# Performance work log

Measured on AMD Instinct MI355X. Metric: run time of the kernel, lower is better.

## Reference

```python
import jax, jax.numpy as jnp
import numpy as np
import math
from jax import lax

KSIZE = 3
STRIDE = 1
RATE = 2
FUSE_K = 3
SCALE = 10.0
FUSE = True


def extract_image_patches(img, kernel, stride=1):
    # Faithful port of the torch helper (incl. pad_row applied to width).
    bsz, c, h, w = img.shape
    h2 = math.ceil(h / stride)
    w2 = math.ceil(w / stride)
    pad_row = (h2 - 1) * stride + kernel - h
    pad_col = (w2 - 1) * stride + kernel - w
    x = jnp.pad(img, ((0, 0), (0, 0),
                      (pad_col // 2, pad_col - pad_col // 2),
                      (pad_row // 2, pad_row - pad_row // 2)))
    H, W = x.shape[2], x.shape[3]
    nh = (H - kernel) // stride + 1
    nw = (W - kernel) // stride + 1
    parts = [x[:, :, ki:ki + (nh - 1) * stride + 1:stride,
                     kj:kj + (nw - 1) * stride + 1:stride]
             for ki in range(kernel) for kj in range(kernel)]
    p = jnp.stack(parts, axis=1)  # [b, k*k, c, nh, nw] -> flatten order (ki,kj,c)
    return p.reshape(bsz, kernel * kernel * c, nh, nw)


def setup_inputs() -> dict:
    key = jax.random.key(0)
    k1, k2 = jax.random.split(key)
    f = jax.random.normal(k1, (2, 64, 128, 128), dtype=jnp.float32)
    b = jax.random.normal(k2, (2, 64, 128, 128), dtype=jnp.float32)
    mask = jnp.zeros((2, 1, 128, 128), dtype=jnp.float32)
    return {"f": f, "b": b, "mask": mask}


def reference(f, b, mask):
    kernel = RATE * 2
    bs, cs, hs, ws = f.shape
    # raw background patches at stride=rate with kernel=2*rate
    raw_w = extract_image_patches(b, kernel, RATE * STRIDE)
    raw_w = raw_w.reshape(bs, -1, kernel, kernel, cs).transpose(0, 1, 4, 2, 3)  # [bs,L,cs,K,K]
    # nearest-neighbor downsample by rate (torch nearest: src = dst*rate)
    f_ds = f[:, :, ::RATE, ::RATE]
    b_ds = b[:, :, ::RATE, ::RATE]
    mask_ds = mask[:, :, ::RATE, ::RATE]
    ihs, iws = b_ds.shape[2], b_ds.shape[3]
    L = ihs * iws
    # ksize x ksize matching patches
    w = extract_image_patches(b_ds, KSIZE, STRIDE)
    w = w.reshape(bs, -1, KSIZE, KSIZE, cs).transpose(0, 1, 4, 2, 3)  # [bs,L,cs,3,3]
    # mask patches -> per-patch validity mm [L]
    m = extract_image_patches(mask_ds, KSIZE, STRIDE)
    m = m.reshape(bs, -1, KSIZE, KSIZE, 1).transpose(0, 2, 3, 4, 1)[0]  # [3,3,1,L]
    mm = (jnp.mean(m, axis=(0, 1, 2)) == 0.0).astype(f.dtype)  # [L]
    fuse_weight = jnp.eye(FUSE_K, dtype=f.dtype).reshape(1, 1, FUSE_K, FUSE_K)

    def per_sample(xi, wi, raw_wi):
        # xi [cs,ihs,iws], wi [L,cs,3,3], raw_wi [L,cs,K,K]
        norm = jnp.sqrt(jnp.sum(wi * wi, axis=(1, 2, 3)))
        wi_normed = wi / jnp.minimum(norm, 1e-4)[:, None, None, None]  # clamp(max=1e-4), faithful
        yi = lax.conv_general_dilated(xi[None], wi_normed, (1, 1), [(1, 1), (1, 1)])  # [1,L,ihs,iws]
        if FUSE:
            yi = yi.reshape(1, 1, ihs * iws, ihs * iws)
            yi = lax.conv_general_dilated(yi, fuse_weight, (1, 1), [(1, 1), (1, 1)])
            yi = yi.reshape(1, ihs, iws, ihs, iws).transpose(0, 2, 1, 4, 3)
            yi = yi.reshape(1, 1, ihs * iws, ihs * iws)
            yi = lax.conv_general_dilated(yi, fuse_weight, (1, 1), [(1, 1), (1, 1)])
            yi = yi.reshape(1, iws, ihs, iws, ihs).transpose(0, 2, 1, 4, 3)
        yi = yi.reshape(1, ihs, iws, iws * ihs)
        yi = jax.nn.softmax(yi * mm * SCALE, axis=3) * mm
        offset = jnp.argmax(yi, axis=3).astype(jnp.int32)
        offset = jnp.stack([offset // hs, offset % hs], axis=-1).transpose(0, 3, 1, 2)  # [1,2,ihs,iws]
        yi_t = yi.transpose(0, 3, 1, 2)  # [1,L,ihs,iws]
        # conv_transpose2d(yi_t, raw_wi, stride=rate, padding=1) via lhs dilation
        w_t = jnp.flip(raw_wi, axis=(-2, -1)).transpose(1, 0, 2, 3)  # [cs,L,K,K]
        pad = kernel - 1 - 1
        out = lax.conv_general_dilated(yi_t, w_t, (1, 1), [(pad, pad), (pad, pad)],
                                       lhs_dilation=(RATE, RATE)) / 4.0  # [1,cs,hs,ws]
        return out[0], offset[0]

    y, offsets = jax.vmap(per_sample)(f_ds, w, raw_w)
    h_add = jnp.broadcast_to(jnp.arange(ihs, dtype=offsets.dtype).reshape(1, 1, ihs, 1), (bs, 1, ihs, iws))
    w_add = jnp.broadcast_to(jnp.arange(iws, dtype=offsets.dtype).reshape(1, 1, 1, iws), (bs, 1, ihs, iws))
    offsets = offsets - jnp.concatenate([h_add, w_add], axis=1)
    return y, offsets
```

## Files before the change

### kernel.cpp

```cpp
#include <hip/hip_runtime.h>
#include <math.h>

#define NS   4096
#define KCH  576
#define CH   64
#define HF   128
#define HD   64
#define PLANE (NS*KCH)
#define IMG  (CH*HF*HF)

typedef __attribute__((ext_vector_type(8))) _Float16 half8;
typedef __attribute__((ext_vector_type(4))) float f32x4;

__device__ __forceinline__ int Tsw(int r){ return ((r & 63) << 6) | (r >> 6); }

typedef __attribute__((address_space(1))) unsigned int gu32;
typedef __attribute__((address_space(3))) unsigned int lu32;
__device__ __forceinline__ void gload16(const void* g, void* l){
  __builtin_amdgcn_global_load_lds((const gu32*)g, (lu32*)l, 16, 0, 0);
}

__global__ void k_mm(const float* __restrict__ mask, float* __restrict__ mm){
  int n = blockIdx.x * blockDim.x + threadIdx.x;
  if(n >= NS) return;
  float sum = 0.f;
  #pragma unroll
  for(int r9 = 0; r9 < 9; ++r9){
    int idx = n * 9 + r9;
    int p   = idx >> 12;
    int rem = idx & 4095;
    int y = rem >> 6, x = rem & 63;
    int ki = p / 3, kj = p % 3;
    int Y = ki + y - 1, X = kj + x - 1;
    float v = 0.f;
    if(Y >= 0 && Y < HD && X >= 0 && X < HD)
      v = mask[(2*Y) * HF + 2*X];
    sum += v;
  }
  mm[n] = ((sum / 9.0f) == 0.0f) ? 1.0f : 0.0f;
}

__global__ void k_WX(const float* __restrict__ f, const float* __restrict__ b,
                     _Float16* __restrict__ Wp, _Float16* __restrict__ Xp){
  int e0 = blockIdx.x * 256 + threadIdx.x;
  int samp = e0 / (2*PLANE);
  int ew = e0 - samp * (2*PLANE);
  const float* fp = f + (size_t)samp * IMG;
  const float* bp = b + (size_t)samp * IMG;
  _Float16* Wps = Wp + (size_t)samp * (2*PLANE);
  _Float16* Xps = Xp + (size_t)samp * (2*PLANE);
  if(ew < PLANE){
    int e = ew;
    int n = e / KCH, k = e - n * KCH;
    int c2 = k / 9, r9 = k - c2 * 9;
    int t = n * 9 + r9;
    int y = t & 63, ch = (t >> 6) & 63, p = t >> 12;
    int ki = p / 3, kj = p - ki * 3;
    int Y = ki + y - 1, X = kj + c2 - 1;
    float v = 0.f;
    if((unsigned)Y < 64u && (unsigned)X < 64u)
      v = bp[ch * (HF*HF) + (Y << 8) + (X << 1)];
    v *= 9.765625f;
    _Float16 h0 = (_Float16)v;
    _Float16 h1 = (_Float16)(v - (float)h0);
    Wps[e] = h0; Wps[PLANE + e] = h1;
  } else {
    int e = ew - PLANE;
    int s = e / KCH, k = e - s * KCH;
    int c2 = k / 9, r9 = k - c2 * 9, a = r9 / 3, bb = r9 - a * 3;
    int i = s >> 6, j = s & 63;
    int Y = i + a - 1, Xc = j + bb - 1;
    float v = 0.f;
    if((unsigned)Y < 64u && (unsigned)Xc < 64u)
      v = fp[c2 * (HF*HF) + (Y << 8) + (Xc << 1)];
    v *= 1024.0f;
    _Float16 h0 = (_Float16)v;
    _Float16 h1 = (_Float16)(v - (float)h0);
    Xps[e] = h0; Xps[PLANE + e] = h1;
  }
}

#define CLUSTER(G,H,BR)                                                          \
  __builtin_amdgcn_s_setprio(1);                                                 \
  _Pragma("unroll")                                                              \
  for(int mf = 0; mf < 4; ++mf)                                                  \
    _Pragma("unroll")                                                            \
    for(int nf = 0; nf < 2; ++nf)                                                \
      _Pragma("unroll")                                                          \
      for(int ks = 0; ks < 2; ++ks)                                              \
        acc[G][mf][H][nf] = __builtin_amdgcn_mfma_f32_16x16x32_f16(              \
            Ar[mf][ks], BR[nf][ks], acc[G][mf][H][nf], 0, 0, 0);                 \
  __builtin_amdgcn_s_setprio(0);

__global__ __launch_bounds__(512, 2) void k_gemm(const _Float16* __restrict__ Wp,
                                                 const _Float16* __restrict__ Xp,
                                                 float* __restrict__ A){
  __shared__ char smem[131072];
  const int tid  = threadIdx.x;
  const int lane = tid & 63, wv = tid >> 6;
  const int wr = wv >> 2, wc = wv & 3;
  const int samp = blockIdx.x >> 8;
  const int bid  = blockIdx.x & 255;
  const _Float16* Wps = Wp + (size_t)samp * (2*PLANE);
  const _Float16* Xps = Xp + (size_t)samp * (2*PLANE);
  float* As = A + (size_t)samp * NS * NS;
  const int xcd = bid & 7, slot = bid >> 3;
  const int bx = ((xcd & 3) << 2) | (slot & 3);
  const int by = ((xcd >> 2) << 3) | (slot >> 2);
  const int bn = by << 8, bs = bx << 8;

  f32x4 acc[2][4][2][2];
  #pragma unroll
  for(int g = 0; g < 2; ++g)
    #pragma unroll
    for(int mf = 0; mf < 4; ++mf)
      #pragma unroll
      for(int h = 0; h < 2; ++h)
        #pragma unroll
        for(int nf = 0; nf < 2; ++nf) acc[g][mf][h][nf] = (f32x4){0.f,0.f,0.f,0.f};

  const int srow = tid >> 3;
  const int sq8  = ((tid & 7) ^ (srow & 7)) << 3;
  const int ldso = tid << 4;

  auto stage = [&](int bufB, int t, int half){
    int term = t / 9;
    int k0 = (t - term * 9) << 6;
    const _Float16* pl;
    int rowbase, ldsbase;
    if(half == 0 || half == 3){
      pl = Wps + (size_t)(term >> 1) * PLANE;
      int g = (half == 3);
      rowbase = bn + (g << 7);
      ldsbase = bufB + (g << 14);
    } else {
      pl = Xps + (size_t)(term & 1) * PLANE;
      int h = (half == 2);
      rowbase = bs + (h << 7);
      ldsbase = bufB + 32768 + (h << 14);
    }
    const _Float16* src = pl + (size_t)(rowbase + srow) * KCH + k0 + sq8;
    gload16(src,            smem + ldsbase + ldso);
    gload16(src + 64*KCH,   smem + ldsbase + 8192 + ldso);
  };

  const int rA  = ((wr << 6) + (lane & 15)) << 7;
  const int rB  = ((wc << 5) + (lane & 15)) << 7;
  const int co0 = (((lane >> 4) ^ (lane & 7)) << 4);

  half8 Ar[4][2], B0r[2][2], B1r[2][2];
  auto readA = [&](int bufB, int g){
    const char* base = smem + bufB + (g << 14) + rA + co0;
    #pragma unroll
    for(int mf = 0; mf < 4; ++mf){
      Ar[mf][0] = *(const half8*)(base + (mf << 11));
      Ar[mf][1] = *(const half8*)(base + (mf << 11) + ((64 ^ co0) - co0));
    }
  };
  auto readB = [&](int bufB, int h, half8 (*Br)[2]){
    const char* base = smem + bufB + 32768 + (h << 14) + rB + co0;
    #pragma unroll
    for(int nf = 0; nf < 2; ++nf){
      Br[nf][0] = *(const half8*)(base + (nf << 11));
      Br[nf][1] = *(const half8*)(base + (nf << 11) + ((64 ^ co0) - co0));
    }
  };

  stage(0, 0, 0); stage(0, 0, 1); stage(0, 0, 2); stage(0, 0, 3);

  for(int t = 0; t < 27; ++t){
    const int bufB  = (t & 1) << 16;
    const int nbufB = bufB ^ 65536;
    const bool more = (t < 26);
    if(more){ stage(nbufB, t+1, 0); asm volatile("s_waitcnt vmcnt(6)" ::: "memory"); }
    else    {                       asm volatile("s_waitcnt vmcnt(4)" ::: "memory"); }
    __builtin_amdgcn_s_barrier(); asm volatile("" ::: "memory");
    readA(bufB, 0); readB(bufB, 0, B0r);
    CLUSTER(0,0,B0r)
    asm volatile("" ::: "memory"); __builtin_amdgcn_s_barrier(); asm volatile("" ::: "memory");
    if(more){ stage(nbufB, t+1, 1); stage(nbufB, t+1, 2);
              asm volatile("s_waitcnt vmcnt(8)" ::: "memory"); }
    else    { asm volatile("s_waitcnt vmcnt(2)" ::: "memory"); }
    __builtin_amdgcn_s_barrier(); asm volatile("" ::: "memory");
    readB(bufB, 1, B1r);
    CLUSTER(0,1,B1r)
    asm volatile("" ::: "memory"); __builtin_amdgcn_s_barrier(); asm volatile("" ::: "memory");
    if(more){ stage(nbufB, t+1, 3); asm volatile("s_waitcnt vmcnt(8)" ::: "memory"); }
    else    {                       asm volatile("s_waitcnt vmcnt(0)" ::: "memory"); }
    __builtin_amdgcn_s_barrier(); asm volatile("" ::: "memory");
    readA(bufB, 1);
    CLUSTER(1,1,B1r)
    CLUSTER(1,0,B0r)
    asm volatile("" ::: "memory"); __builtin_amdgcn_s_barrier(); asm volatile("" ::: "memory");
  }

  #pragma unroll
  for(int g = 0; g < 2; ++g)
    #pragma unroll
    for(int mf = 0; mf < 4; ++mf){
      int row0 = bn + (g << 7) + (wr << 6) + (mf << 4) + ((lane >> 4) << 2);
      #pragma unroll
      for(int h = 0; h < 2; ++h)
        #pragma unroll
        for(int nf = 0; nf < 2; ++nf){
          int col = bs + (h << 7) + (wc << 5) + (nf << 4) + (lane & 15);
          #pragma unroll
          for(int r = 0; r < 4; ++r)
            As[((size_t)(row0 + r) << 12) + col] = acc[g][mf][h][nf][r];
        }
    }
}

__global__ __launch_bounds__(256) void k_f1(const float* __restrict__ A,
                                            float* __restrict__ B){
  const int n = ((blockIdx.x & 7) << 9) | (blockIdx.x >> 3);
  const int tid = threadIdx.x;
  const float* r0 = A + ((size_t)n << 12);
  const float* rm = r0 - 4096;
  const float* rp = r0 + 4096;
  const bool vm = (n >= 1), vp = (n <= 4094);
  float* Bw = B + ((size_t)n << 12);
  const float4 z4 = {0.f, 0.f, 0.f, 0.f};
  #pragma unroll
  for(int it = 0; it < 4; ++it){
    int cb = ((it << 8) + tid) << 2;
    float4 f0 = *(const float4*)(r0 + cb);
    float4 fm = vm ? *(const float4*)(rm + cb) : z4;
    float4 fp = vp ? *(const float4*)(rp + cb) : z4;
    float sm = (vm && cb > 0)    ? rm[cb - 1] : 0.f;
    float sp = (vp && cb < 4092) ? rp[cb + 4] : 0.f;
    float4 o;
    {
      float t0 = sm;           t0 += f0.x; t0 += fp.y;               o.x = t0;
      float t1 = fm.x;         t1 += f0.y; t1 += fp.z;               o.y = t1;
      float t2 = fm.y;         t2 += f0.z; t2 += fp.w;               o.z = t2;
      float t3 = fm.z;         t3 += f0.w; t3 += sp;                 o.w = t3;
    }
    *(float4*)(Bw + cb) = o;
  }
}

__global__ __launch_bounds__(256) void k_f2(const float* __restrict__ B,
                                            const float* __restrict__ mm,
                                            int* __restrict__ cnt, int* __restrict__ cand_s,
                                            float* __restrict__ cand_w,
                                            float* __restrict__ out_off){
  const int tn = ((blockIdx.x & 7) << 9) | (blockIdx.x >> 3);
  const int n  = Tsw(tn);
  const int tid = threadIdx.x;
  __shared__ float f1[256];
  __shared__ int   i1[256];
  __shared__ float s_max, s_sum;
  __shared__ int   s_cnt, s_cs[16];
  __shared__ float s_ce[16];

  const bool v2m = (tn >= 1), v2p = (tn <= 4094);
  const float* Rm = B + ((size_t)(v2m ? Tsw(tn - 1) : 0) << 12);
  const float* R0 = B + ((size_t)n << 12);
  const float* Rp = B + ((size_t)(v2p ? Tsw(tn + 1) : 0) << 12);

  const int wv = tid >> 6, ln = tid & 63;

  float z[16];
  #pragma unroll
  for(int r = 0; r < 16; ++r){
    int s = tid + (r << 8);
    int a = (r << 2) + wv;
    float tm = 0.f;
    if(v2m){
      if(a >= 1)            tm = Rm[s - 64];
      else if(ln >= 1)      tm = Rm[4031 + ln];
    }
    float t = tm;
    t += R0[s];
    float tp = 0.f;
    if(v2p){
      if(a <= 62)           tp = Rp[s + 64];
      else if(ln <= 62)     tp = Rp[ln + 1];
    }
    t += tp;
    z[r] = t;
  }

  float mmv[16];
  float lm = -3.4e38f;
  #pragma unroll
  for(int r = 0; r < 16; ++r){
    mmv[r] = mm[tid + (r << 8)];
    z[r] = z[r] * mmv[r] * 10.0f;
    lm = fmaxf(lm, z[r]);
  }
  f1[tid] = lm; __syncthreads();
  for(int st = 128; st > 0; st >>= 1){ if(tid < st) f1[tid] = fmaxf(f1[tid], f1[tid+st]); __syncthreads(); }
  if(tid == 0){ s_max = f1[0]; s_cnt = 0; }
  __syncthreads();
  float mx = s_max;

  float sum = 0.f, best = -1.0f; int bidx = 0;
  #pragma unroll
  for(int r = 0; r < 16; ++r){
    float d = z[r] - mx;
    float e = 0.f;
    if(__any(d > -20.0f)) e = expf(d);
    sum += e;
    float pe = e * mmv[r];
    int s = tid + (r << 8);
    if(pe > best){ best = pe; bidx = s; }
    if(pe > 1e-6f){
      int sl = atomicAdd(&s_cnt, 1);
      if(sl < 16){ s_cs[sl] = s; s_ce[sl] = pe; }
    }
  }
  f1[tid] = sum; __syncthreads();
  for(int st = 128; st > 0; st >>= 1){ if(tid < st) f1[tid] += f1[tid+st]; __syncthreads(); }
  if(tid == 0) s_sum = f1[0];
  __syncthreads();

  f1[tid] = best; i1[tid] = bidx; __syncthreads();
  for(int st = 128; st > 0; st >>= 1){
    if(tid < st){
      float v2 = f1[tid+st]; int j2 = i1[tid+st];
      if(v2 > f1[tid] || (v2 == f1[tid] && j2 < i1[tid])){ f1[tid] = v2; i1[tid] = j2; }
    }
    __syncthreads();
  }
  if(tid == 0){
    int sA = i1[0]; float vA = f1[0];
    int sBest = (vA > 0.0f) ? sA : 0;
    int c = min(s_cnt, 16);
    if(vA > 0.0f){
      bool found = false;
      for(int q = 0; q < c; ++q) if(s_cs[q] == sA) found = true;
      if(!found){ if(c < 16){ s_cs[c] = sA; s_ce[c] = vA; ++c; } else { s_cs[0] = sA; s_ce[0] = vA; } }
    }
    cnt[n] = c;
    float inv = 1.0f / s_sum;
    for(int q = 0; q < c; ++q){ cand_s[n*16+q] = s_cs[q]; cand_w[n*16+q] = s_ce[q] * inv; }
    out_off[n]      = (float)((sBest >> 7)  - (n >> 6));
    out_off[NS + n] = (float)((sBest & 127) - (n & 63));
  }
}

__global__ __launch_bounds__(256) void k_y(const float* __restrict__ bp,
                    const int* __restrict__ cnt, const int* __restrict__ cand_s,
                    const float* __restrict__ cand_w, float* __restrict__ outy){
  __shared__ float lv[16 * 65];
  const int sb  = blockIdx.x;
  const int oy  = sb >> 3;
  const int ox0 = (sb & 7) << 4;
  const int co  = threadIdx.x & 63, pq = threadIdx.x >> 6;
  const int kyp = oy & 1;
  const int xb  = 2 * co - 1;

  #pragma unroll
  for(int rr = 0; rr < 4; ++rr){
    const int px = (pq << 2) + rr;
    const int ox = ox0 + px;
    const int kxp = ox & 1;
    float val = 0.f;
    #pragma unroll
    for(int ia = 0; ia < 2; ++ia){
      int ky = kyp + 2*ia;
      int un = oy + ky - 2;
      if(un < 0 || un > 126) continue;
      int u = un >> 1;
      #pragma unroll
      for(int ib = 0; ib < 2; ++ib){
        int kx = kxp + 2*ib;
        int vn = ox + kx - 2;
        if(vn < 0 || vn > 126) continue;
        int v = vn >> 1;
        int n = (u << 6) | v;
        int c = cnt[n];
        int ky2 = 3 - ky, kx2 = 3 - kx;
        for(int q = 0; q < c; ++q){
          int s = cand_s[n*16 + q];
          float w = cand_w[n*16 + q];
          int p = s >> 8, ki = p >> 2, kj = p & 3, ch = (s >> 2) & 63;
          int Y = ((s & 3) << 4) + (ky2 << 2) + kx2;
          int yy = ki + 2*Y - 1;
          int xx = kj + xb;
          if(yy >= 0 && yy < HF && (unsigned)xx < (unsigned)HF)
            val += w * bp[(ch << 14) + (yy << 7) + xx];
        }
      }
    }
    lv[px * 65 + co] = val * 0.25f;
  }
  __syncthreads();
  const int pxw = threadIdx.x & 15;
  const int cw0 = threadIdx.x >> 4;
  #pragma unroll
  for(int it = 0; it < 4; ++it){
    int c2 = cw0 + (it << 4);
    outy[(c2 << 14) + (oy << 7) + ox0 + pxw] = lv[pxw * 65 + c2];
  }
}

extern "C" void kernel_launch(void* const* d_in, const int* in_sizes, int n_in,
                              void* d_out, int out_size, void* d_ws, size_t ws_size,
                              hipStream_t stream){
  const float* f    = (const float*)d_in[0];
  const float* b    = (const float*)d_in[1];
  const float* mask = (const float*)d_in[2];
  float* out = (float*)d_out;
  char* ws = (char*)d_ws;

  const size_t SEMI_WS = 201883648ull;
  if(ws_size >= SEMI_WS){
    float*    A      = (float*)(ws);
    _Float16* Wp     = (_Float16*)(ws + 134217728ull);
    _Float16* Xp     = (_Float16*)(ws + 153092096ull);
    float*    Bf     = (float*)(ws + 134217728ull);
    float*    mmv    = (float*)(ws + 201326592ull);
    int*      cntv   = (int*)  (ws + 201342976ull);
    int*      cand_s = (int*)  (ws + 201359360ull);
    float*    cand_w = (float*)(ws + 201621504ull);

    k_mm<<<16, 256, 0, stream>>>(mask, mmv);
    k_WX<<<(4*PLANE)/256, 256, 0, stream>>>(f, b, Wp, Xp);
    k_gemm<<<512, 512, 0, stream>>>(Wp, Xp, A);
    for(int s = 0; s < 2; ++s){
      const float* bp = b + (size_t)s * IMG;
      k_f1<<<4096, 256, 0, stream>>>(A + (size_t)s * NS * NS, Bf);
      k_f2<<<4096, 256, 0, stream>>>(Bf, mmv, cntv, cand_s, cand_w,
                                     out + 2*IMG + s*2*NS);
      k_y<<<1024, 256, 0, stream>>>(bp, cntv, cand_s, cand_w,
                                    out + (size_t)s * IMG);
    }
  } else {
    float*     A      = (float*)(ws);
    float*     Bf     = (float*)(ws + 67108864ull);
    _Float16*  Wp     = (_Float16*)(ws + 134217728ull);
    _Float16*  Xp     = (_Float16*)(ws + 143654912ull);
    float*     mmv    = (float*)(ws + 153092096ull);
    int*       cntv   = (int*)  (ws + 153108480ull);
    int*       cand_s = (int*)  (ws + 153124864ull);
    float*     cand_w = (float*)(ws + 153387008ull);

    k_mm<<<16, 256, 0, stream>>>(mask, mmv);
    for(int s = 0; s < 2; ++s){
      const float* fp = f + (size_t)s * IMG;
      const float* bp = b + (size_t)s * IMG;
      k_WX<<<(2*PLANE)/256, 256, 0, stream>>>(fp, bp, Wp, Xp);
      k_gemm<<<256, 512, 0, stream>>>(Wp, Xp, A);
      k_f1<<<4096, 256, 0, stream>>>(A, Bf);
      k_f2<<<4096, 256, 0, stream>>>(Bf, mmv, cntv, cand_s, cand_w,
                                     out + 2*IMG + s*2*NS);
      k_y<<<1024, 256, 0, stream>>>(bp, cntv, cand_s, cand_w,
                                    out + (size_t)s * IMG);
    }
  }
}
```

Baseline: 300.2 us.

## Batch both samples into single f1/f2/y launches and use wave-shuffle reductions

```diff
diff --git a/kernel.cpp b/kernel.cpp
--- a/kernel.cpp
+++ b/kernel.cpp
@@ -213,13 +213,17 @@
 
 __global__ __launch_bounds__(256) void k_f1(const float* __restrict__ A,
                                             float* __restrict__ B){
-  const int n = ((blockIdx.x & 7) << 9) | (blockIdx.x >> 3);
+  const int samp = blockIdx.x >> 12;
+  const int sbid = blockIdx.x & 4095;
+  const int n = ((sbid & 7) << 9) | (sbid >> 3);
   const int tid = threadIdx.x;
-  const float* r0 = A + ((size_t)n << 12);
+  const float* As = A + (size_t)samp * NS * NS;
+  float* Bs = B + (size_t)samp * NS * NS;
+  const float* r0 = As + ((size_t)n << 12);
   const float* rm = r0 - 4096;
   const float* rp = r0 + 4096;
   const bool vm = (n >= 1), vp = (n <= 4094);
-  float* Bw = B + ((size_t)n << 12);
+  float* Bw = Bs + ((size_t)n << 12);
   const float4 z4 = {0.f, 0.f, 0.f, 0.f};
   #pragma unroll
   for(int it = 0; it < 4; ++it){
@@ -245,19 +249,25 @@
                                             int* __restrict__ cnt, int* __restrict__ cand_s,
                                             float* __restrict__ cand_w,
                                             float* __restrict__ out_off){
-  const int tn = ((blockIdx.x & 7) << 9) | (blockIdx.x >> 3);
+  const int samp = blockIdx.x >> 12;
+  const int sbid = blockIdx.x & 4095;
+  const int tn = ((sbid & 7) << 9) | (sbid >> 3);
   const int n  = Tsw(tn);
   const int tid = threadIdx.x;
-  __shared__ float f1[256];
-  __shared__ int   i1[256];
-  __shared__ float s_max, s_sum;
+  const float* Bs = B + (size_t)samp * NS * NS;
+  int* cnts = cnt + samp * NS;
+  int* cand_ss = cand_s + samp * NS * 16;
+  float* cand_ws = cand_w + samp * NS * 16;
+  float* oo = out_off + samp * 2 * NS;
+  __shared__ float fw[4];
+  __shared__ int   iw[4];
   __shared__ int   s_cnt, s_cs[16];
   __shared__ float s_ce[16];
 
   const bool v2m = (tn >= 1), v2p = (tn <= 4094);
-  const float* Rm = B + ((size_t)(v2m ? Tsw(tn - 1) : 0) << 12);
-  const float* R0 = B + ((size_t)n << 12);
-  const float* Rp = B + ((size_t)(v2p ? Tsw(tn + 1) : 0) << 12);
+  const float* Rm = Bs + ((size_t)(v2m ? Tsw(tn - 1) : 0) << 12);
+  const float* R0 = Bs + ((size_t)n << 12);
+  const float* Rp = Bs + ((size_t)(v2p ? Tsw(tn + 1) : 0) << 12);
 
   const int wv = tid >> 6, ln = tid & 63;
 
@@ -290,11 +300,12 @@
     z[r] = z[r] * mmv[r] * 10.0f;
     lm = fmaxf(lm, z[r]);
   }
-  f1[tid] = lm; __syncthreads();
-  for(int st = 128; st > 0; st >>= 1){ if(tid < st) f1[tid] = fmaxf(f1[tid], f1[tid+st]); __syncthreads(); }
-  if(tid == 0){ s_max = f1[0]; s_cnt = 0; }
+  #pragma unroll
+  for(int off = 32; off > 0; off >>= 1) lm = fmaxf(lm, __shfl_xor(lm, off));
+  if(ln == 0) fw[wv] = lm;
+  if(tid == 0) s_cnt = 0;
   __syncthreads();
-  float mx = s_max;
+  const float mx = fmaxf(fmaxf(fw[0], fw[1]), fmaxf(fw[2], fw[3]));
 
   float sum = 0.f, best = -1.0f; int bidx = 0;
   #pragma unroll
@@ -311,21 +322,29 @@
       if(sl < 16){ s_cs[sl] = s; s_ce[sl] = pe; }
     }
   }
-  f1[tid] = sum; __syncthreads();
-  for(int st = 128; st > 0; st >>= 1){ if(tid < st) f1[tid] += f1[tid+st]; __syncthreads(); }
-  if(tid == 0) s_sum = f1[0];
+  #pragma unroll
+  for(int off = 32; off > 0; off >>= 1) sum += __shfl_xor(sum, off);
+  if(ln == 0) fw[wv] = sum;
   __syncthreads();
-
-  f1[tid] = best; i1[tid] = bidx; __syncthreads();
-  for(int st = 128; st > 0; st >>= 1){
-    if(tid < st){
-      float v2 = f1[tid+st]; int j2 = i1[tid+st];
-      if(v2 > f1[tid] || (v2 == f1[tid] && j2 < i1[tid])){ f1[tid] = v2; i1[tid] = j2; }
-    }
-    __syncthreads();
-  }
+  const float s_sum = fw[0] + fw[1] + fw[2] + fw[3];
+  __syncthreads();
+
+  #pragma unroll
+  for(int off = 32; off > 0; off >>= 1){
+    float ov = __shfl_xor(best, off);
+    int   oi = __shfl_xor(bidx, off);
+    if(ov > best || (ov == best && oi < bidx)){ best = ov; bidx = oi; }
+  }
+  if(ln == 0){ fw[wv] = best; iw[wv] = bidx; }
+  __syncthreads();
+
   if(tid == 0){
-    int sA = i1[0]; float vA = f1[0];
+    float vA = fw[0]; int sA = iw[0];
+    #pragma unroll
+    for(int q = 1; q < 4; ++q){
+      float v2 = fw[q]; int j2 = iw[q];
+      if(v2 > vA || (v2 == vA && j2 < sA)){ vA = v2; sA = j2; }
+    }
     int sBest = (vA > 0.0f) ? sA : 0;
     int c = min(s_cnt, 16);
     if(vA > 0.0f){
@@ -333,19 +352,25 @@
       for(int q = 0; q < c; ++q) if(s_cs[q] == sA) found = true;
       if(!found){ if(c < 16){ s_cs[c] = sA; s_ce[c] = vA; ++c; } else { s_cs[0] = sA; s_ce[0] = vA; } }
     }
-    cnt[n] = c;
+    cnts[n] = c;
     float inv = 1.0f / s_sum;
-    for(int q = 0; q < c; ++q){ cand_s[n*16+q] = s_cs[q]; cand_w[n*16+q] = s_ce[q] * inv; }
-    out_off[n]      = (float)((sBest >> 7)  - (n >> 6));
-    out_off[NS + n] = (float)((sBest & 127) - (n & 63));
-  }
-}
-
-__global__ __launch_bounds__(256) void k_y(const float* __restrict__ bp,
+    for(int q = 0; q < c; ++q){ cand_ss[n*16+q] = s_cs[q]; cand_ws[n*16+q] = s_ce[q] * inv; }
+    oo[n]      = (float)((sBest >> 7)  - (n >> 6));
+    oo[NS + n] = (float)((sBest & 127) - (n & 63));
+  }
+}
+
+__global__ __launch_bounds__(256) void k_y(const float* __restrict__ b,
                     const int* __restrict__ cnt, const int* __restrict__ cand_s,
                     const float* __restrict__ cand_w, float* __restrict__ outy){
   __shared__ float lv[16 * 65];
-  const int sb  = blockIdx.x;
+  const int samp = blockIdx.x >> 10;
+  const int sb  = blockIdx.x & 1023;
+  const float* bp = b + (size_t)samp * IMG;
+  const int* cnts = cnt + samp * NS;
+  const int* cand_ss = cand_s + samp * NS * 16;
+  const float* cand_ws = cand_w + samp * NS * 16;
+  float* oys = outy + (size_t)samp * IMG;
   const int oy  = sb >> 3;
   const int ox0 = (sb & 7) << 4;
   const int co  = threadIdx.x & 63, pq = threadIdx.x >> 6;
@@ -371,11 +396,11 @@
         if(vn < 0 || vn > 126) continue;
         int v = vn >> 1;
         int n = (u << 6) | v;
-        int c = cnt[n];
+        int c = cnts[n];
         int ky2 = 3 - ky, kx2 = 3 - kx;
         for(int q = 0; q < c; ++q){
-          int s = cand_s[n*16 + q];
-          float w = cand_w[n*16 + q];
+          int s = cand_ss[n*16 + q];
+          float w = cand_ws[n*16 + q];
           int p = s >> 8, ki = p >> 2, kj = p & 3, ch = (s >> 2) & 63;
           int Y = ((s & 3) << 4) + (ky2 << 2) + kx2;
           int yy = ki + 2*Y - 1;
@@ -393,7 +418,7 @@
   #pragma unroll
   for(int it = 0; it < 4; ++it){
     int c2 = cw0 + (it << 4);
-    outy[(c2 << 14) + (oy << 7) + ox0 + pxw] = lv[pxw * 65 + c2];
+    oys[(c2 << 14) + (oy << 7) + ox0 + pxw] = lv[pxw * 65 + c2];
   }
 }
 
@@ -406,8 +431,26 @@
   float* out = (float*)d_out;
   char* ws = (char*)d_ws;
 
+  const size_t FULL_WS = 269512704ull;
   const size_t SEMI_WS = 201883648ull;
-  if(ws_size >= SEMI_WS){
+
+  if(ws_size >= FULL_WS){
+    float*    A      = (float*)(ws);
+    _Float16* Wp     = (_Float16*)(ws + 134217728ull);
+    _Float16* Xp     = (_Float16*)(ws + 153092096ull);
+    float*    Bf     = (float*)(ws + 134217728ull);
+    float*    mmv    = (float*)(ws + 268435456ull);
+    int*      cntv   = (int*)  (ws + 268451840ull);
+    int*      cand_s = (int*)  (ws + 268484608ull);
+    float*    cand_w = (float*)(ws + 269008896ull);
+
+    k_mm<<<16, 256, 0, stream>>>(mask, mmv);
+    k_WX<<<(4*PLANE)/256, 256, 0, stream>>>(f, b, Wp, Xp);
+    k_gemm<<<512, 512, 0, stream>>>(Wp, Xp, A);
+    k_f1<<<8192, 256, 0, stream>>>(A, Bf);
+    k_f2<<<8192, 256, 0, stream>>>(Bf, mmv, cntv, cand_s, cand_w, out + 2*IMG);
+    k_y<<<2048, 256, 0, stream>>>(b, cntv, cand_s, cand_w, out);
+  } else if(ws_size >= SEMI_WS){
     float*    A      = (float*)(ws);
     _Float16* Wp     = (_Float16*)(ws + 134217728ull);
     _Float16* Xp     = (_Float16*)(ws + 153092096ull);
```

New measurement: 294.8 us, median of 2. No clear change (-1.8%).
